# Performance work log

Measured on AMD Instinct MI355X. Metric: run time of the kernel, lower is better.

The kernel has to match this reference:

```python
import jax, jax.numpy as jnp
import numpy as np

H = 16  # n_heads

def setup_inputs() -> dict:
    key = jax.random.key(0)
    ks = jax.random.split(key, 11)
    B, L, D = 2, 2048, 1024
    w = 1.0 / np.sqrt(D).astype(np.float32)
    return {
        "query": jax.random.normal(ks[0], (B, L, D), jnp.float32),
        "key":   jax.random.normal(ks[1], (B, L, D), jnp.float32),
        "value": jax.random.normal(ks[2], (B, L, D), jnp.float32),
        "Wq": jax.random.normal(ks[3], (D, D), jnp.float32) * w,
        "bq": jax.random.normal(ks[4], (D,), jnp.float32) * 0.01,
        "Wk": jax.random.normal(ks[5], (D, D), jnp.float32) * w,
        "bk": jax.random.normal(ks[6], (D,), jnp.float32) * 0.01,
        "Wv": jax.random.normal(ks[7], (D, D), jnp.float32) * w,
        "bv": jax.random.normal(ks[8], (D,), jnp.float32) * 0.01,
        "Wo": jax.random.normal(ks[9], (D, D), jnp.float32) * w,
        "bo": jax.random.normal(ks[10], (D,), jnp.float32) * 0.01,
        "masksize": 256,
    }

def reference(query, key, value, Wq, bq, Wk, bk, Wv, bv, Wo, bo, masksize):
    B, L, D = query.shape
    d_k = D // H
    scale = 1.0 / np.sqrt(d_k).astype(np.float32)

    def proj(x, W, b):
        # nn.Linear: x @ W.T + b, then [B,L,H,d_k] -> [B,H,L,d_k]
        return (x @ W.T + b).reshape(B, L, H, d_k).transpose(0, 2, 1, 3)

    q = proj(query, Wq, bq)
    k = proj(key, Wk, bk)
    v = proj(value, Wv, bv)

    # Sliding-window float mask (faithful to original: a 0/1 FLOAT tensor is
    # passed as attn_mask to SDPA, so it is ADDED to scores, not -inf-masked).
    half = masksize // 2
    i = jnp.arange(L)[:, None]
    j = jnp.arange(L)[None, :]
    band = (jnp.abs(i - j) <= half).astype(q.dtype)  # [L, L]

    scores = jnp.einsum('bhqd,bhkd->bhqk', q, k) * scale + band  # [B,H,L,L]
    attn = jax.nn.softmax(scores, axis=-1)
    out = jnp.einsum('bhqk,bhkd->bhqd', attn, v)  # [B,H,L,d_k]
    out = out.transpose(0, 2, 1, 3).reshape(B, L, D)
    return out @ Wo.T + bo
```

## Files before the change

kernel.cpp:

```cpp
#include <hip/hip_runtime.h>
#include <hip/hip_bf16.h>

#define Hh 16
#define Ll 2048
#define Dd 1024
#define DK 64
#define Mm 4096
#define Kk 1024
#define Nn 1024

typedef short bf16x8 __attribute__((ext_vector_type(8)));
typedef float f32x4 __attribute__((ext_vector_type(4)));

static __device__ __forceinline__ unsigned short f2bf(float f) {
    union { __hip_bfloat16 b; unsigned short u; } cv;
    cv.b = __float2bfloat16(f);
    return cv.u;
}

static __device__ __forceinline__ unsigned packtr(float a, float b) {
    return __builtin_amdgcn_perm(__builtin_bit_cast(unsigned, b),
                                 __builtin_bit_cast(unsigned, a), 0x07060302u);
}

static __device__ __forceinline__ float fexp2(float x) {
    return __builtin_amdgcn_exp2f(x);
}

static __device__ __forceinline__ void glds16(const ushort* g, ushort* l) {
    __builtin_amdgcn_global_load_lds((const __attribute__((address_space(1))) unsigned int*)g,
                                     (__attribute__((address_space(3))) unsigned int*)l,
                                     16, 0, 0);
}

__global__ __launch_bounds__(256) void cast_all(
    const float* __restrict__ q, const float* __restrict__ k, const float* __restrict__ v,
    const float* __restrict__ wq, const float* __restrict__ wk, const float* __restrict__ wv,
    const float* __restrict__ wo,
    ushort* __restrict__ qb, ushort* __restrict__ kb, ushort* __restrict__ vb,
    ushort* __restrict__ wqb, ushort* __restrict__ wkb, ushort* __restrict__ wvb,
    ushort* __restrict__ wob) {
    const int bx = blockIdx.x;
    const float4* s; ushort4* d; int base;
    if      (bx <  4096) { s = (const float4*)q;  d = (ushort4*)qb;  base = 0; }
    else if (bx <  8192) { s = (const float4*)k;  d = (ushort4*)kb;  base = 4096; }
    else if (bx < 12288) { s = (const float4*)v;  d = (ushort4*)vb;  base = 8192; }
    else if (bx < 13312) { s = (const float4*)wq; d = (ushort4*)wqb; base = 12288; }
    else if (bx < 14336) { s = (const float4*)wk; d = (ushort4*)wkb; base = 13312; }
    else if (bx < 15360) { s = (const float4*)wv; d = (ushort4*)wvb; base = 14336; }
    else                 { s = (const float4*)wo; d = (ushort4*)wob; base = 15360; }
    const int i = (bx - base) * 256 + threadIdx.x;
    float4 vv = s[i];
    ushort4 o;
    o.x = f2bf(vv.x); o.y = f2bf(vv.y); o.z = f2bf(vv.z); o.w = f2bf(vv.w);
    d[i] = o;
}

__global__ __launch_bounds__(256) void gemm_qkv(
    const ushort* __restrict__ A0, const ushort* __restrict__ A1, const ushort* __restrict__ A2,
    const ushort* __restrict__ W0, const ushort* __restrict__ W1, const ushort* __restrict__ W2,
    const float* __restrict__ b0, const float* __restrict__ b1, const float* __restrict__ b2,
    ushort* __restrict__ O0, ushort* __restrict__ O1, ushort* __restrict__ OVt) {
    __shared__ __align__(16) ushort SM[2 * 128 * 64];
    ushort* As = SM;
    ushort* Bs = SM + 8192;

    const int fl = blockIdx.x;
    const int xcd = fl & 7, bcoli = (fl >> 3) & 7, slot = fl >> 6;
    const int g = slot * 8 + xcd;
    const int z = g >> 5;
    const int browi = g & 31;

    const ushort* A = (z == 0) ? A0 : (z == 1) ? A1 : A2;
    const ushort* W = (z == 0) ? W0 : (z == 1) ? W1 : W2;
    const float* bias = (z == 0) ? b0 : (z == 1) ? b1 : b2;

    const int t = threadIdx.x;
    const int wave = t >> 6, lane = t & 63;
    const int quad = lane >> 4, l15 = lane & 15;
    const int brow = browi * 128, bcol = bcoli * 128;
    const int wr = (wave >> 1) * 64, wc = (wave & 1) * 64;
    const int sr = lane >> 3;
    const int sg = ((lane & 7) ^ sr) * 8;

    f32x4 acc[4][4] = {};

    for (int k0 = 0; k0 < Kk; k0 += 64) {
        __syncthreads();
#pragma unroll
        for (int c = 0; c < 4; c++) {
            const int row = wave * 32 + c * 8;
            glds16(A + (size_t)(brow + row + sr) * Kk + k0 + sg, As + row * 64);
            glds16(W + (size_t)(bcol + row + sr) * Kk + k0 + sg, Bs + row * 64);
        }
        __syncthreads();

        bf16x8 af[2][4], bfr[2][4];
#pragma unroll
        for (int kk = 0; kk < 2; kk++) {
            const int pos8 = (((kk * 4 + quad) ^ (l15 & 7)) * 8);
#pragma unroll
            for (int i = 0; i < 4; i++)
                af[kk][i] = *(const bf16x8*)(As + (wr + i * 16 + l15) * 64 + pos8);
#pragma unroll
            for (int j = 0; j < 4; j++)
                bfr[kk][j] = *(const bf16x8*)(Bs + (wc + j * 16 + l15) * 64 + pos8);
        }
#pragma unroll
        for (int kk = 0; kk < 2; kk++)
#pragma unroll
            for (int i = 0; i < 4; i++)
#pragma unroll
                for (int j = 0; j < 4; j++)
                    acc[i][j] = __builtin_amdgcn_mfma_f32_16x16x32_bf16(af[kk][i], bfr[kk][j], acc[i][j], 0, 0, 0);
    }

    if (z < 2) {
        ushort* Out = (z == 0) ? O0 : O1;
        const float oscl = (z == 0) ? 0.18033688f : 1.0f;
        const int b = brow >> 11;
        const int lbase = (brow & 2047) + wr;
        const int h = (bcol + wc) >> 6;
        ushort* T = SM + wave * 1280;
        __syncthreads();
#pragma unroll
        for (int i = 0; i < 4; i++) {
#pragma unroll
            for (int j = 0; j < 4; j++) {
                const float bv = bias[bcol + wc + j * 16 + l15];
#pragma unroll
                for (int r = 0; r < 4; r++)
                    T[(quad * 4 + r) * 80 + j * 16 + l15] = f2bf((acc[i][j][r] + bv) * oscl);
            }
            const int r8 = lane >> 3, c8 = lane & 7;
#pragma unroll
            for (int pass = 0; pass < 2; pass++) {
                const uint4 val = *(const uint4*)(T + (pass * 8 + r8) * 80 + c8 * 8);
                const int l = lbase + i * 16 + pass * 8 + r8;
                *(uint4*)(Out + ((size_t)(b * Hh + h) * Ll + l) * DK + c8 * 8) = val;
            }
        }
    } else {
        ushort* T = SM;
        const int b = brow >> 11;
        const int lbase = brow & 2047;
        const int npr = (wave & 1) * 16 + l15;
#pragma unroll
        for (int j = 0; j < 4; j++) {
            __syncthreads();
            const float bv = bias[bcol + wc + j * 16 + l15];
#pragma unroll
            for (int i = 0; i < 4; i++)
#pragma unroll
                for (int r = 0; r < 4; r++) {
                    const int m = wr + i * 16 + quad * 4 + r;
                    T[npr * 136 + m] = f2bf(acc[i][j][r] + bv);
                }
            __syncthreads();
#pragma unroll
            for (int cc = 0; cc < 2; cc++) {
                const int idx = t + cc * 256;
                const int ni = idx >> 4;
                const int ms = idx & 15;
                const int n = bcol + (ni >> 4) * 64 + j * 16 + (ni & 15);
                const int hh = n >> 6, dk = n & 63;
                uint4 val = *(const uint4*)(T + ni * 136 + ms * 8);
                *(uint4*)(OVt + ((size_t)(b * Hh + hh) * DK + dk) * Ll + lbase + ms * 8) = val;
            }
        }
    }
}

__global__ __launch_bounds__(256, 2) void attn_kernel(const ushort* __restrict__ Q,
                                                      const ushort* __restrict__ Kp,
                                                      const ushort* __restrict__ Vt,
                                                      ushort* __restrict__ Oout,
                                                      const int* __restrict__ masksize) {
    __shared__ __align__(16) ushort SM[32768];
    const int t = threadIdx.x;
    const int wave = t >> 6, lane = t & 63;
    const int quad = lane >> 4, l15 = lane & 15;
    const int bx = blockIdx.x;
    const int bh = bx & 31, qc = bx >> 5;
    const int q0w = qc * 128 + wave * 32;
    const int half = masksize[0] >> 1;
    const unsigned wid = (unsigned)(2 * half);

    const ushort* Qb = Q + (size_t)bh * (Ll * DK);
    const ushort* Kb = Kp + (size_t)bh * (Ll * DK);
    const ushort* Vb = Vt + (size_t)bh * (DK * Ll);

    const bf16x8 qA0 = *(const bf16x8*)(Qb + (size_t)(q0w + l15) * DK + quad * 8);
    const bf16x8 qA1 = *(const bf16x8*)(Qb + (size_t)(q0w + l15) * DK + 32 + quad * 8);
    const bf16x8 qB0 = *(const bf16x8*)(Qb + (size_t)(q0w + 16 + l15) * DK + quad * 8);
    const bf16x8 qB1 = *(const bf16x8*)(Qb + (size_t)(q0w + 16 + l15) * DK + 32 + quad * 8);

    const float C2IN  = (1.0f - 24.0f) * 1.44269504088896f;
    const float C2OUT = -24.0f * 1.44269504088896f;
    const float E1 = 2.718281828f;

    bf16x8 onesf;
#pragma unroll
    for (int j = 0; j < 8; j++) onesf[j] = (short)0x3F80;

    f32x4 OA0[4] = {}, OB0[4] = {}, OA1[4] = {}, OB1[4] = {};
    f32x4 SA0 = {}, SB0 = {}, SA1 = {}, SB1 = {};

    const int krow = lane >> 2;
    const int kcol8 = (((lane & 3) ^ ((lane >> 3) & 3)) * 8);
    const int qsw8 = (quad ^ ((l15 >> 1) & 3)) * 8;
    const int vd8 = lane >> 3;
    const int vgp = 2 * (lane & 7);

#define STAGE_J(J, BUF)                                                                    \
    do {                                                                                   \
        const int kt0_ = (J) * 64, kt1_ = 1024 + (J) * 64;                                 \
        if (wave < 2) {                                                                    \
            const int ktk_ = (wave == 0) ? kt0_ : kt1_;                                    \
            ushort* dst_ = SM + wave * 8192 + (BUF) * 4096;                                \
            _Pragma("unroll")                                                              \
            for (int c_ = 0; c_ < 4; c_++)                                                 \
                _Pragma("unroll")                                                          \
                for (int pan_ = 0; pan_ < 2; pan_++)                                       \
                    glds16(Kb + (size_t)(ktk_ + c_ * 16 + krow) * DK + pan_ * 32 + kcol8,  \
                           dst_ + pan_ * 2048 + c_ * 512);                                 \
        } else {                                                                           \
            const int ktv_ = (wave == 2) ? kt0_ : kt1_;                                    \
            ushort* dst_ = SM + 16384 + (wave - 2) * 8192 + (BUF) * 4096;                  \
            _Pragma("unroll")                                                              \
            for (int s_ = 0; s_ < 8; s_++) {                                               \
                const int d_ = s_ * 8 + vd8;                                               \
                glds16(Vb + (size_t)d_ * Ll + ktv_ + ((vgp ^ (d_ & 14)) * 4),              \
                       dst_ + s_ * 512);                                                   \
            }                                                                              \
        }                                                                                  \
    } while (0)

#define STREAM_BODY(KB, VB, KT, CV, OAx, OBx, SAx, SBx, UNIF)                              \
    _Pragma("unroll")                                                                      \
    for (int s = 0; s < 2; s++) {                                                          \
        const bf16x8 kf00 = *(const bf16x8*)((KB) + ((2 * s) * 16 + l15) * 32 + qsw8);     \
        const bf16x8 kf01 = *(const bf16x8*)((KB) + 2048 + ((2 * s) * 16 + l15) * 32 + qsw8); \
        const bf16x8 kf10 = *(const bf16x8*)((KB) + ((2 * s + 1) * 16 + l15) * 32 + qsw8); \
        const bf16x8 kf11 = *(const bf16x8*)((KB) + 2048 + ((2 * s + 1) * 16 + l15) * 32 + qsw8); \
        f32x4 zA0 = __builtin_amdgcn_mfma_f32_16x16x32_bf16(kf00, qA0, (CV), 0, 0, 0);     \
        zA0 = __builtin_amdgcn_mfma_f32_16x16x32_bf16(kf01, qA1, zA0, 0, 0, 0);            \
        f32x4 zA1 = __builtin_amdgcn_mfma_f32_16x16x32_bf16(kf10, qA0, (CV), 0, 0, 0);     \
        zA1 = __builtin_amdgcn_mfma_f32_16x16x32_bf16(kf11, qA1, zA1, 0, 0, 0);            \
        f32x4 zB0 = __builtin_amdgcn_mfma_f32_16x16x32_bf16(kf00, qB0, (CV), 0, 0, 0);     \
        zB0 = __builtin_amdgcn_mfma_f32_16x16x32_bf16(kf01, qB1, zB0, 0, 0, 0);            \
        f32x4 zB1 = __builtin_amdgcn_mfma_f32_16x16x32_bf16(kf10, qB0, (CV), 0, 0, 0);     \
        zB1 = __builtin_amdgcn_mfma_f32_16x16x32_bf16(kf11, qB1, zB1, 0, 0, 0);            \
        float pA[8], pB[8];                                                                \
        if (UNIF) {                                                                        \
            _Pragma("unroll")                                                              \
            for (int g = 0; g < 2; g++)                                                    \
                _Pragma("unroll")                                                          \
                for (int r = 0; r < 4; r++) {                                              \
                    pA[g * 4 + r] = fexp2(g ? zA1[r] : zA0[r]);                            \
                    pB[g * 4 + r] = fexp2(g ? zB1[r] : zB0[r]);                            \
                }                                                                          \
        } else {                                                                           \
            const int kb = (KT) + s * 32 + quad * 4 + half;                                \
            _Pragma("unroll")                                                              \
            for (int g = 0; g < 2; g++)                                                    \
                _Pragma("unroll")                                                          \
                for (int r = 0; r < 4; r++) {                                              \
                    const unsigned ttA = (unsigned)(kb + g * 16 + r - (q0w + l15));        \
                    const unsigned ttB = (unsigned)(kb + g * 16 + r - (q0w + 16 + l15));   \
                    pA[g * 4 + r] = fexp2(g ? zA1[r] : zA0[r]) * (ttA <= wid ? E1 : 1.0f); \
                    pB[g * 4 + r] = fexp2(g ? zB1[r] : zB0[r]) * (ttB <= wid ? E1 : 1.0f); \
                }                                                                          \
        }                                                                                  \
        bf16x8 pfA, pfB;                                                                   \
        ((unsigned*)&pfA)[0] = packtr(pA[0], pA[1]);                                       \
        ((unsigned*)&pfA)[1] = packtr(pA[2], pA[3]);                                       \
        ((unsigned*)&pfA)[2] = packtr(pA[4], pA[5]);                                       \
        ((unsigned*)&pfA)[3] = packtr(pA[6], pA[7]);                                       \
        ((unsigned*)&pfB)[0] = packtr(pB[0], pB[1]);                                       \
        ((unsigned*)&pfB)[1] = packtr(pB[2], pB[3]);                                       \
        ((unsigned*)&pfB)[2] = packtr(pB[4], pB[5]);                                       \
        ((unsigned*)&pfB)[3] = packtr(pB[6], pB[7]);                                       \
        SAx = __builtin_amdgcn_mfma_f32_16x16x32_bf16(pfA, onesf, SAx, 0, 0, 0);           \
        SBx = __builtin_amdgcn_mfma_f32_16x16x32_bf16(pfB, onesf, SBx, 0, 0, 0);           \
        _Pragma("unroll")                                                                  \
        for (int i = 0; i < 4; i++) {                                                      \
            const int bi = (i * 16 + l15) * 64;                                            \
            const int x14 = l15 & 14;                                                      \
            const ushort4 v1 = *(const ushort4*)((VB) + bi + (((s * 8 + quad) ^ x14) * 4)); \
            const ushort4 v2 = *(const ushort4*)((VB) + bi + (((s * 8 + 4 + quad) ^ x14) * 4)); \
            bf16x8 vc;                                                                     \
            *(ushort4*)&vc = v1;                                                           \
            *((ushort4*)&vc + 1) = v2;                                                     \
            OAx[i] = __builtin_amdgcn_mfma_f32_16x16x32_bf16(pfA, vc, OAx[i], 0, 0, 0);    \
            OBx[i] = __builtin_amdgcn_mfma_f32_16x16x32_bf16(pfB, vc, OBx[i], 0, 0, 0);    \
        }                                                                                  \
    }

    STAGE_J(0, 0);
    int cur = 0;
    const int qlo = q0w, qhi = q0w + 31;

    for (int j = 0; j < 16; ++j) {
        const int kt0 = j * 64, kt1 = 1024 + j * 64;
        __syncthreads();
        if (j < 15) STAGE_J(j + 1, cur ^ 1);

        const ushort* K0b = SM + cur * 4096;
        const ushort* K1b = SM + 8192 + cur * 4096;
        const ushort* V0b = SM + 16384 + cur * 4096;
        const ushort* V1b = SM + 24576 + cur * 4096;

        const bool allout0 = (kt0 + 63 < qlo - half) || (kt0 > qhi + half);
        const bool allin0  = (kt0 >= qhi - half) && (kt0 + 63 <= qlo + half);
        const bool allout1 = (kt1 + 63 < qlo - half) || (kt1 > qhi + half);
        const bool allin1  = (kt1 >= qhi - half) && (kt1 + 63 <= qlo + half);

        if ((allin0 || allout0) && (allin1 || allout1)) {
            const float c0 = allin0 ? C2IN : C2OUT;
            const float c1 = allin1 ? C2IN : C2OUT;
            const f32x4 cv0 = {c0, c0, c0, c0};
            const f32x4 cv1 = {c1, c1, c1, c1};
            STREAM_BODY(K0b, V0b, kt0, cv0, OA0, OB0, SA0, SB0, 1);
            STREAM_BODY(K1b, V1b, kt1, cv1, OA1, OB1, SA1, SB1, 1);
        } else {
            const f32x4 cvo = {C2OUT, C2OUT, C2OUT, C2OUT};
            STREAM_BODY(K0b, V0b, kt0, cvo, OA0, OB0, SA0, SB0, 0);
            STREAM_BODY(K1b, V1b, kt1, cvo, OA1, OB1, SA1, SB1, 0);
        }
        cur ^= 1;
    }
#undef STAGE_J
#undef STREAM_BODY

    float liA[4], liB[4];
#pragma unroll
    for (int r = 0; r < 4; r++) {
        liA[r] = 1.0f / (SA0[r] + SA1[r]);
        liB[r] = 1.0f / (SB0[r] + SB1[r]);
    }

    const int b = bh >> 4, h = bh & 15;
#pragma unroll
    for (int i = 0; i < 4; i++)
#pragma unroll
        for (int r = 0; r < 4; r++) {
            const int qa = q0w + quad * 4 + r;
            Oout[((size_t)b * Ll + qa) * Dd + h * DK + i * 16 + l15] =
                f2bf((OA0[i][r] + OA1[i][r]) * liA[r]);
            Oout[((size_t)b * Ll + qa + 16) * Dd + h * DK + i * 16 + l15] =
                f2bf((OB0[i][r] + OB1[i][r]) * liB[r]);
        }
}

__global__ __launch_bounds__(256) void gemm_o(const ushort* __restrict__ A,
                                              const ushort* __restrict__ W,
                                              const float* __restrict__ bias,
                                              float* __restrict__ Out) {
    __shared__ __align__(16) ushort SM[2 * 128 * 64];
    ushort* As = SM;
    ushort* Bs = SM + 8192;
    const int fl = blockIdx.x;
    const int xcd = fl & 7, bcoli = (fl >> 3) & 7, slot = fl >> 6;
    const int browi = slot * 8 + xcd;
    const int t = threadIdx.x;
    const int wave = t >> 6, lane = t & 63;
    const int quad = lane >> 4, l15 = lane & 15;
    const int brow = browi * 128, bcol = bcoli * 128;
    const int wr = (wave >> 1) * 64, wc = (wave & 1) * 64;
    const int sr = lane >> 3;
    const int sg = ((lane & 7) ^ sr) * 8;

    f32x4 acc[4][4] = {};

    for (int k0 = 0; k0 < Kk; k0 += 64) {
        __syncthreads();
#pragma unroll
        for (int c = 0; c < 4; c++) {
            const int row = wave * 32 + c * 8;
            glds16(A + (size_t)(brow + row + sr) * Kk + k0 + sg, As + row * 64);
            glds16(W + (size_t)(bcol + row + sr) * Kk + k0 + sg, Bs + row * 64);
        }
        __syncthreads();

        bf16x8 af[2][4], bfr[2][4];
#pragma unroll
        for (int kk = 0; kk < 2; kk++) {
            const int pos8 = (((kk * 4 + quad) ^ (l15 & 7)) * 8);
#pragma unroll
            for (int i = 0; i < 4; i++)
                af[kk][i] = *(const bf16x8*)(As + (wr + i * 16 + l15) * 64 + pos8);
#pragma unroll
            for (int j = 0; j < 4; j++)
                bfr[kk][j] = *(const bf16x8*)(Bs + (wc + j * 16 + l15) * 64 + pos8);
        }
#pragma unroll
        for (int kk = 0; kk < 2; kk++)
#pragma unroll
            for (int i = 0; i < 4; i++)
#pragma unroll
                for (int j = 0; j < 4; j++)
                    acc[i][j] = __builtin_amdgcn_mfma_f32_16x16x32_bf16(af[kk][i], bfr[kk][j], acc[i][j], 0, 0, 0);
    }

#pragma unroll
    for (int i = 0; i < 4; i++)
#pragma unroll
        for (int j = 0; j < 4; j++) {
            const int n = bcol + wc + j * 16 + l15;
            const float bv = bias[n];
#pragma unroll
            for (int r = 0; r < 4; r++) {
                const int m = brow + wr + i * 16 + quad * 4 + r;
                Out[(size_t)m * Nn + n] = acc[i][j][r] + bv;
            }
        }
}

extern "C" void kernel_launch(void* const* d_in, const int* in_sizes, int n_in,
                              void* d_out, int out_size, void* d_ws, size_t ws_size,
                              hipStream_t stream) {
    const float* query = (const float*)d_in[0];
    const float* key   = (const float*)d_in[1];
    const float* value = (const float*)d_in[2];
    const float* Wq = (const float*)d_in[3];
    const float* bq = (const float*)d_in[4];
    const float* Wk = (const float*)d_in[5];
    const float* bk = (const float*)d_in[6];
    const float* Wv = (const float*)d_in[7];
    const float* bv = (const float*)d_in[8];
    const float* Wo = (const float*)d_in[9];
    const float* bo = (const float*)d_in[10];
    const int* masksize = (const int*)d_in[11];

    char* ws = (char*)d_ws;
    const size_t MB = 1024 * 1024;
    ushort* qb  = (ushort*)(ws + 0 * MB);
    ushort* kbf = (ushort*)(ws + 8 * MB);
    ushort* vbf = (ushort*)(ws + 16 * MB);
    ushort* wqb = (ushort*)(ws + 24 * MB);
    ushort* wkb = (ushort*)(ws + 26 * MB);
    ushort* wvb = (ushort*)(ws + 28 * MB);
    ushort* wob = (ushort*)(ws + 30 * MB);
    ushort* Qp  = (ushort*)(ws + 32 * MB);
    ushort* Kp  = (ushort*)(ws + 40 * MB);
    ushort* Vt  = (ushort*)(ws + 48 * MB);
    ushort* AO  = (ushort*)(ws + 56 * MB);

    cast_all<<<16384, 256, 0, stream>>>(query, key, value, Wq, Wk, Wv, Wo,
                                        qb, kbf, vbf, wqb, wkb, wvb, wob);

    gemm_qkv<<<768, 256, 0, stream>>>(qb, kbf, vbf,
                                      wqb, wkb, wvb,
                                      bq, bk, bv,
                                      Qp, Kp, Vt);

    attn_kernel<<<512, 256, 0, stream>>>(Qp, Kp, Vt, AO, masksize);

    gemm_o<<<256, 256, 0, stream>>>(AO, wob, bo, (float*)d_out);
}
```

Measured before the change: 225.2 us.

## Double-buffer LDS tiles in QKV and output projection GEMMs

Both projection GEMM kernels now use two LDS buffers. The global-to-LDS load for the next K tile is issued before computing on the current one, and one barrier per iteration replaces two. The goal is to hide global memory latency behind the MFMA work. The cost is twice the LDS per block, which can lower occupancy, and the overlap only holds if the compiler does not insert a full wait before the LDS reads.

```diff
diff --git a/kernel.cpp b/kernel.cpp
--- a/kernel.cpp
+++ b/kernel.cpp
@@ -61,9 +61,7 @@
     const ushort* __restrict__ W0, const ushort* __restrict__ W1, const ushort* __restrict__ W2,
     const float* __restrict__ b0, const float* __restrict__ b1, const float* __restrict__ b2,
     ushort* __restrict__ O0, ushort* __restrict__ O1, ushort* __restrict__ OVt) {
-    __shared__ __align__(16) ushort SM[2 * 128 * 64];
-    ushort* As = SM;
-    ushort* Bs = SM + 8192;
+    __shared__ __align__(16) ushort SM[2 * 16384];
 
     const int fl = blockIdx.x;
     const int xcd = fl & 7, bcoli = (fl >> 3) & 7, slot = fl >> 6;
@@ -85,15 +83,27 @@
 
     f32x4 acc[4][4] = {};
 
+#define QSTAGE(K0, BUF)                                                                    \
+    do {                                                                                   \
+        ushort* As_ = SM + (BUF) * 16384;                                                  \
+        ushort* Bs_ = SM + (BUF) * 16384 + 8192;                                           \
+        _Pragma("unroll")                                                                  \
+        for (int c_ = 0; c_ < 4; c_++) {                                                   \
+            const int row_ = wave * 32 + c_ * 8;                                           \
+            glds16(A + (size_t)(brow + row_ + sr) * Kk + (K0) + sg, As_ + row_ * 64);      \
+            glds16(W + (size_t)(bcol + row_ + sr) * Kk + (K0) + sg, Bs_ + row_ * 64);      \
+        }                                                                                  \
+    } while (0)
+
+    QSTAGE(0, 0);
+    int cur = 0;
+
     for (int k0 = 0; k0 < Kk; k0 += 64) {
         __syncthreads();
-#pragma unroll
-        for (int c = 0; c < 4; c++) {
-            const int row = wave * 32 + c * 8;
-            glds16(A + (size_t)(brow + row + sr) * Kk + k0 + sg, As + row * 64);
-            glds16(W + (size_t)(bcol + row + sr) * Kk + k0 + sg, Bs + row * 64);
-        }
-        __syncthreads();
+        if (k0 + 64 < Kk) QSTAGE(k0 + 64, cur ^ 1);
+
+        const ushort* As = SM + cur * 16384;
+        const ushort* Bs = SM + cur * 16384 + 8192;
 
         bf16x8 af[2][4], bfr[2][4];
 #pragma unroll
@@ -113,7 +123,9 @@
 #pragma unroll
                 for (int j = 0; j < 4; j++)
                     acc[i][j] = __builtin_amdgcn_mfma_f32_16x16x32_bf16(af[kk][i], bfr[kk][j], acc[i][j], 0, 0, 0);
-    }
+        cur ^= 1;
+    }
+#undef QSTAGE
 
     if (z < 2) {
         ushort* Out = (z == 0) ? O0 : O1;
@@ -357,9 +369,7 @@
                                               const ushort* __restrict__ W,
                                               const float* __restrict__ bias,
                                               float* __restrict__ Out) {
-    __shared__ __align__(16) ushort SM[2 * 128 * 64];
-    ushort* As = SM;
-    ushort* Bs = SM + 8192;
+    __shared__ __align__(16) ushort SM[2 * 16384];
     const int fl = blockIdx.x;
     const int xcd = fl & 7, bcoli = (fl >> 3) & 7, slot = fl >> 6;
     const int browi = slot * 8 + xcd;
@@ -373,15 +383,27 @@
 
     f32x4 acc[4][4] = {};
 
+#define OSTAGE(K0, BUF)                                                                    \
+    do {                                                                                   \
+        ushort* As_ = SM + (BUF) * 16384;                                                  \
+        ushort* Bs_ = SM + (BUF) * 16384 + 8192;                                           \
+        _Pragma("unroll")                                                                  \
+        for (int c_ = 0; c_ < 4; c_++) {                                                   \
+            const int row_ = wave * 32 + c_ * 8;                                           \
+            glds16(A + (size_t)(brow + row_ + sr) * Kk + (K0) + sg, As_ + row_ * 64);      \
+            glds16(W + (size_t)(bcol + row_ + sr) * Kk + (K0) + sg, Bs_ + row_ * 64);      \
+        }                                                                                  \
+    } while (0)
+
+    OSTAGE(0, 0);
+    int cur = 0;
+
     for (int k0 = 0; k0 < Kk; k0 += 64) {
         __syncthreads();
-#pragma unroll
-        for (int c = 0; c < 4; c++) {
-            const int row = wave * 32 + c * 8;
-            glds16(A + (size_t)(brow + row + sr) * Kk + k0 + sg, As + row * 64);
-            glds16(W + (size_t)(bcol + row + sr) * Kk + k0 + sg, Bs + row * 64);
-        }
-        __syncthreads();
+        if (k0 + 64 < Kk) OSTAGE(k0 + 64, cur ^ 1);
+
+        const ushort* As = SM + cur * 16384;
+        const ushort* Bs = SM + cur * 16384 + 8192;
 
         bf16x8 af[2][4], bfr[2][4];
 #pragma unroll
@@ -401,7 +423,9 @@
 #pragma unroll
                 for (int j = 0; j < 4; j++)
                     acc[i][j] = __builtin_amdgcn_mfma_f32_16x16x32_bf16(af[kk][i], bfr[kk][j], acc[i][j], 0, 0, 0);
-    }
+        cur ^= 1;
+    }
+#undef OSTAGE
 
 #pragma unroll
     for (int i = 0; i < 4; i++)
```

Result: faster. 206.9 us (-8.1%).
